# Performance work log

Hardware: AMD Instinct MI355X
Metric: run time of the kernel (lower is better)

## Reference

```python
import math
import jax, jax.numpy as jnp
import numpy as np

B, S, T = 32, 512, 180
D, F, L, H = 512, 2048, 6, 8
DH = D // H


def _pos_encoding(length, d):
    pos = np.arange(length, dtype=np.float32)[:, None]
    div = np.exp(np.arange(0, d, 2, dtype=np.float32) * (-math.log(10000.0) / d))
    pe = np.zeros((length, d), dtype=np.float32)
    pe[:, 0::2] = np.sin(pos * div)
    pe[:, 1::2] = np.cos(pos * div)
    return jnp.asarray(pe)


def _ln(x, scale, bias):
    mu = x.mean(-1, keepdims=True)
    var = ((x - mu) ** 2).mean(-1, keepdims=True)
    return (x - mu) * jax.lax.rsqrt(var + 1e-5) * scale + bias


def _mha(q_in, kv_in, w, b, causal=False):
    # w: [4, D, D] = (Wq, Wk, Wv, Wo); b: [4, D]
    b_, sq = q_in.shape[:2]
    q = (q_in @ w[0] + b[0]).reshape(b_, sq, H, DH)
    k = (kv_in @ w[1] + b[1]).reshape(b_, -1, H, DH)
    v = (kv_in @ w[2] + b[2]).reshape(b_, -1, H, DH)
    s = jnp.einsum('bqhd,bkhd->bhqk', q, k) / math.sqrt(DH)
    if causal:
        mask = jnp.tril(jnp.ones((sq, k.shape[1]), dtype=bool))
        s = jnp.where(mask, s, -1e9)
    a = jax.nn.softmax(s, axis=-1)
    o = jnp.einsum('bhqk,bkhd->bqhd', a, v).reshape(b_, sq, D)
    return o @ w[3] + b[3]


def _ffn(x, w1, b1, w2, b2):
    return jax.nn.relu(x @ w1 + b1) @ w2 + b2


def setup_inputs() -> dict:
    key = jax.random.key(0)
    ks = jax.random.split(key, 16)
    n = lambda k, shape: jax.random.normal(k, shape, jnp.float32) * 0.02
    return {
        'x': jax.random.normal(ks[0], (B, S, 2), jnp.float32),
        'y_cv_teacher': jax.random.normal(ks[1], (B, T, 1), jnp.float32),
        'src_proj_w': n(ks[2], (2, D)), 'src_proj_b': jnp.zeros((D,), jnp.float32),
        'tgt_proj_w': n(ks[3], (1, D)), 'tgt_proj_b': jnp.zeros((D,), jnp.float32),
        'enc_attn_w': n(ks[4], (L, 4, D, D)), 'enc_attn_b': jnp.zeros((L, 4, D), jnp.float32),
        'enc_ffn_w1': n(ks[5], (L, D, F)), 'enc_ffn_b1': jnp.zeros((L, F), jnp.float32),
        'enc_ffn_w2': n(ks[6], (L, F, D)), 'enc_ffn_b2': jnp.zeros((L, D), jnp.float32),
        'enc_ln_scale': jnp.ones((L, 2, D), jnp.float32), 'enc_ln_bias': jnp.zeros((L, 2, D), jnp.float32),
        'dec_self_w': n(ks[7], (L, 4, D, D)), 'dec_self_b': jnp.zeros((L, 4, D), jnp.float32),
        'dec_cross_w': n(ks[8], (L, 4, D, D)), 'dec_cross_b': jnp.zeros((L, 4, D), jnp.float32),
        'dec_ffn_w1': n(ks[9], (L, D, F)), 'dec_ffn_b1': jnp.zeros((L, F), jnp.float32),
        'dec_ffn_w2': n(ks[10], (L, F, D)), 'dec_ffn_b2': jnp.zeros((L, D), jnp.float32),
        'dec_ln_scale': jnp.ones((L, 3, D), jnp.float32), 'dec_ln_bias': jnp.zeros((L, 3, D), jnp.float32),
        'out_w': n(ks[11], (D, 1)), 'out_b': jnp.zeros((1,), jnp.float32),
    }


def reference(x, y_cv_teacher, src_proj_w, src_proj_b, tgt_proj_w, tgt_proj_b,
              enc_attn_w, enc_attn_b, enc_ffn_w1, enc_ffn_b1, enc_ffn_w2, enc_ffn_b2,
              enc_ln_scale, enc_ln_bias, dec_self_w, dec_self_b, dec_cross_w, dec_cross_b,
              dec_ffn_w1, dec_ffn_b1, dec_ffn_w2, dec_ffn_b2, dec_ln_scale, dec_ln_bias,
              out_w, out_b):
    pe = _pos_encoding(512, D)
    # encoder (post-norm, relu FFN, dropout disabled = eval semantics)
    h = x @ src_proj_w + src_proj_b + pe[: x.shape[1]]
    for i in range(L):
        h = _ln(h + _mha(h, h, enc_attn_w[i], enc_attn_b[i]), enc_ln_scale[i, 0], enc_ln_bias[i, 0])
        h = _ln(h + _ffn(h, enc_ffn_w1[i], enc_ffn_b1[i], enc_ffn_w2[i], enc_ffn_b2[i]),
                enc_ln_scale[i, 1], enc_ln_bias[i, 1])
    memory = h
    # teacher-forced decoder input: [start=0, y_cv_teacher[:-1]]
    tgt_in = jnp.concatenate([jnp.zeros((x.shape[0], 1, 1), x.dtype), y_cv_teacher[:, :-1, :]], axis=1)
    d = tgt_in @ tgt_proj_w + tgt_proj_b + pe[: tgt_in.shape[1]]
    for i in range(L):
        d = _ln(d + _mha(d, d, dec_self_w[i], dec_self_b[i], causal=True),
                dec_ln_scale[i, 0], dec_ln_bias[i, 0])
        d = _ln(d + _mha(d, memory, dec_cross_w[i], dec_cross_b[i]),
                dec_ln_scale[i, 1], dec_ln_bias[i, 1])
        d = _ln(d + _ffn(d, dec_ffn_w1[i], dec_ffn_b1[i], dec_ffn_w2[i], dec_ffn_b2[i]),
                dec_ln_scale[i, 2], dec_ln_bias[i, 2])
    return d @ out_w + out_b  # [B, T, 1]
```

## Files before the change

kernel.cpp:

```cpp
#include <hip/hip_runtime.h>
#include <math.h>

#define B_  32
#define S_  512
#define T_  180
#define D_  512
#define F_  2048
#define L_  6
#define H_  8
#define DH_ 64

typedef unsigned short u16;
typedef __attribute__((ext_vector_type(8))) short short8;
typedef __attribute__((ext_vector_type(4))) float floatx4;

__device__ __forceinline__ float bf2f(u16 h) {
    union { unsigned u; float f; } un; un.u = ((unsigned)h) << 16; return un.f;
}
__device__ __forceinline__ u16 f2bf(float f) {
    union { float f; unsigned u; } un; un.f = f;
    unsigned u = un.u;
    u += 0x7fffu + ((u >> 16) & 1u);
    return (u16)(u >> 16);
}
__device__ __forceinline__ unsigned cvt_pk_bf16(float lo, float hi) {
    unsigned r;
    asm("v_cvt_pk_bf16_f32 %0, %1, %2" : "=v"(r) : "v"(lo), "v"(hi));
    return r;
}

__device__ __forceinline__ void gload16(const u16* g, u16* l) {
    __builtin_amdgcn_global_load_lds(
        (const __attribute__((address_space(1))) void*)g,
        (__attribute__((address_space(3))) void*)l, 16, 0, 0);
}

__device__ __forceinline__ float pos_enc(int pos, int c) {
    int i2 = c & ~1;
    float div = expf(-(float)i2 * (9.210340371976184f / 512.0f));
    float arg = (float)pos * div;
    return (c & 1) ? cosf(arg) : sinf(arg);
}

__global__ __launch_bounds__(256) void embed_src_kernel(
    const float* __restrict__ x, const float* __restrict__ w,
    const float* __restrict__ b, u16* __restrict__ h)
{
    int idx = blockIdx.x * 256 + threadIdx.x;
    if (idx >= B_ * S_ * D_) return;
    int c  = idx & (D_ - 1);
    int bs = idx >> 9;
    int s  = bs & (S_ - 1);
    float x0 = x[bs * 2 + 0];
    float x1 = x[bs * 2 + 1];
    h[idx] = f2bf(x0 * w[c] + x1 * w[D_ + c] + b[c] + pos_enc(s, c));
}

__global__ __launch_bounds__(256) void embed_tgt_kernel(
    const float* __restrict__ y, const float* __restrict__ w,
    const float* __restrict__ b, u16* __restrict__ d)
{
    int idx = blockIdx.x * 256 + threadIdx.x;
    if (idx >= B_ * T_ * D_) return;
    int c  = idx & (D_ - 1);
    int bt = idx >> 9;
    int t  = bt % T_;
    int bb = bt / T_;
    float tv = (t == 0) ? 0.0f : y[bb * T_ + (t - 1)];
    d[idx] = f2bf(tv * w[c] + b[c] + pos_enc(t, c));
}

__global__ __launch_bounds__(256) void wconv_kernel(
    const float* __restrict__ W, u16* __restrict__ Wt, int K, int N)
{
    __shared__ float tile[32][33];
    size_t mat = (size_t)blockIdx.z * K * N;
    const float* Wm = W + mat;
    u16* Wtm = Wt + mat;
    int n0 = blockIdx.x * 32, k0 = blockIdx.y * 32;
    int tx = threadIdx.x & 31, ty = threadIdx.x >> 5;
#pragma unroll
    for (int i = 0; i < 32; i += 8)
        tile[ty + i][tx] = Wm[(size_t)(k0 + ty + i) * N + n0 + tx];
    __syncthreads();
#pragma unroll
    for (int i = 0; i < 32; i += 8)
        Wtm[(size_t)(n0 + ty + i) * K + k0 + tx] = f2bf(tile[tx][ty + i]);
}

__global__ __launch_bounds__(256) void gemm_bf16_kernel(
    const u16* __restrict__ A, int lda, const u16* __restrict__ Bt,
    const float* __restrict__ bias, u16* __restrict__ C, int ldc,
    int M, int N, int K, int relu)
{
    __shared__ u16 smem[18432];
    u16* As = smem;
    u16* Bs = smem + 8192;

    int tid  = threadIdx.x;
    int w    = tid >> 6;
    int lane = tid & 63;
    int m0 = blockIdx.y << 7, n0 = blockIdx.x << 7;

    int sr = w * 32 + (lane >> 2);
    int sk = (lane & 3) * 8;
    const u16* ag0 = A  + (size_t)(m0 + sr)      * lda + sk;
    const u16* ag1 = A  + (size_t)(m0 + sr + 16) * lda + sk;
    const u16* bg0 = Bt + (size_t)(n0 + sr)      * K + sk;
    const u16* bg1 = Bt + (size_t)(n0 + sr + 16) * K + sk;
    u16* al0 = As + (w * 2 + 0) * 512;
    u16* al1 = As + (w * 2 + 1) * 512;
    u16* bl0 = Bs + (w * 2 + 0) * 512;
    u16* bl1 = Bs + (w * 2 + 1) * 512;

    int wm = (w >> 1) * 64, wn = (w & 1) * 64;
    int fr = lane & 15;
    int fk = (lane >> 4) * 8;

    floatx4 acc[4][4] = {};

    for (int k0 = 0; k0 < K; k0 += 64) {
#pragma unroll
        for (int hh = 0; hh < 2; ++hh) {
            int go = k0 + hh * 32;
            int lo = hh * 4096;
            gload16(ag0 + go, al0 + lo);
            gload16(ag1 + go, al1 + lo);
            gload16(bg0 + go, bl0 + lo);
            gload16(bg1 + go, bl1 + lo);
        }
        __syncthreads();

#pragma unroll
        for (int hh = 0; hh < 2; ++hh) {
            int lo = hh * 4096;
            short8 af[4], bf[4];
#pragma unroll
            for (int i = 0; i < 4; ++i)
                af[i] = *(const short8*)&As[lo + (wm + i * 16 + fr) * 32 + fk];
#pragma unroll
            for (int j = 0; j < 4; ++j)
                bf[j] = *(const short8*)&Bs[lo + (wn + j * 16 + fr) * 32 + fk];
#pragma unroll
            for (int i = 0; i < 4; ++i)
#pragma unroll
                for (int j = 0; j < 4; ++j)
                    acc[i][j] = __builtin_amdgcn_mfma_f32_16x16x32_bf16(
                        af[i], bf[j], acc[i][j], 0, 0, 0);
        }
        __syncthreads();
    }

    u16* epi = smem + w * 4608;
    int cc = lane & 15;
    int rq = (lane >> 4) * 4;
#pragma unroll
    for (int j = 0; j < 4; ++j) {
        float bj = bias[n0 + wn + j * 16 + cc];
#pragma unroll
        for (int i = 0; i < 4; ++i) {
#pragma unroll
            for (int r = 0; r < 4; ++r) {
                float vv = acc[i][j][r] + bj;
                if (relu) vv = fmaxf(vv, 0.f);
                epi[(i * 16 + rq + r) * 72 + j * 16 + cc] = f2bf(vv);
            }
        }
    }
    __syncthreads();
#pragma unroll
    for (int t = 0; t < 8; ++t) {
        int er = t * 8 + (lane >> 3);
        int ec = (lane & 7) * 8;
        short8 vv = *(const short8*)&epi[er * 72 + ec];
        *(short8*)&C[(size_t)(m0 + wm + er) * ldc + n0 + wn + ec] = vv;
    }
}

#define SBAR()       asm volatile("s_barrier" ::: "memory")
#define WAIT_LGKM0() do { asm volatile("s_waitcnt lgkmcnt(0)" ::: "memory"); \
                          __builtin_amdgcn_sched_barrier(0); } while (0)
#define WAIT_VM(N)   asm volatile("s_waitcnt vmcnt(" #N ")" ::: "memory")

#define RD_A(BUF, MH) do { \
  _Pragma("unroll") for (int i_ = 0; i_ < 4; ++i_) \
  _Pragma("unroll") for (int h_ = 0; h_ < 2; ++h_) \
    a[i_][h_] = *(const short8*)&smem[(BUF) * 16384 + \
        ((MH) * 128 + qm + i_ * 16 + fr) * 64 + cSwz[h_]]; \
} while (0)

#define RD_B(BUF, NH) do { \
  _Pragma("unroll") for (int n_ = 0; n_ < 2; ++n_) \
  _Pragma("unroll") for (int h_ = 0; h_ < 2; ++h_) \
    bb[n_][h_] = *(const short8*)&smem[32768 + (BUF) * 16384 + \
        ((NH) * 128 + qn + n_ * 16 + fr) * 64 + cSwz[h_]]; \
} while (0)

#define PH_MMA(MH, NH) do { \
  __builtin_amdgcn_s_setprio(1); \
  _Pragma("unroll") for (int i_ = 0; i_ < 4; ++i_) \
  _Pragma("unroll") for (int n_ = 0; n_ < 2; ++n_) \
  _Pragma("unroll") for (int h_ = 0; h_ < 2; ++h_) \
    acc[MH][NH][i_][n_] = __builtin_amdgcn_mfma_f32_16x16x32_bf16( \
        a[i_][h_], bb[n_][h_], acc[MH][NH][i_][n_], 0, 0, 0); \
  __builtin_amdgcn_s_setprio(0); \
} while (0)

__global__ __launch_bounds__(512, 2) void gemm256_bf16_kernel(
    const u16* __restrict__ A, int lda, const u16* __restrict__ Bt,
    const float* __restrict__ bias, u16* __restrict__ C, int ldc,
    int M, int N, int K, int relu)
{
    __shared__ __align__(128) u16 smem[65536];
    const int AB0 = 0, AB1 = 16384, BB0 = 32768, BB1 = 49152;

    int tid = threadIdx.x;
    int w = tid >> 6, lane = tid & 63;
    int fr = lane & 15, q = lane >> 4;
    int qm = (w >> 2) * 64, qn = (w & 3) * 32;
    int r8 = tid >> 3;
    int ksrc = (((tid & 7) ^ (r8 & 7)) << 3);
    int cSwz[2];
    cSwz[0] = ((q ^ (fr & 7)) << 3);
    cSwz[1] = (((4 | q) ^ (fr & 7)) << 3);

    int nbx = gridDim.x;
    int nwg = nbx * gridDim.y;
    int flat = blockIdx.y * nbx + blockIdx.x;
    int qq = nwg >> 3, rr = nwg & 7;
    int xcd = flat & 7, sidx = flat >> 3;
    int wg = (xcd < rr ? xcd * (qq + 1) : rr * (qq + 1) + (xcd - rr) * qq) + sidx;
    int m0 = (wg / nbx) << 8, n0 = (wg % nbx) << 8;

    auto stg = [&](const u16* __restrict__ G, int ld, int row0, int bufOff,
                   int half, int gk) {
#pragma unroll
        for (int j = 0; j < 2; ++j) {
            int rl = half * 128 + j * 64 + r8;
            gload16(G + (size_t)(row0 + rl) * ld + gk + ksrc,
                    smem + bufOff + ((half * 128 + j * 64 + (w << 3)) << 6));
        }
    };

    short8 a[4][2], bb[2][2];
    floatx4 acc[2][2][4][2] = {};

    stg(A,  lda, m0, AB0, 0, 0);
    stg(A,  lda, m0, AB0, 1, 0);
    stg(Bt, K,   n0, BB0, 0, 0);
    stg(Bt, K,   n0, BB0, 1, 0);
    stg(Bt, K,   n0, BB1, 1, 64);
    stg(A,  lda, m0, AB1, 1, 64);
    WAIT_VM(4);
    SBAR();

    int NIT = K >> 7;
    for (int it = 0; it < NIT; ++it) {
        const int notlast = (it < NIT - 1);
        const int gk1 = it * 128 + 64, gk2 = gk1 + 64, gk3 = gk2 + 64;
        RD_A(0, 0); RD_B(0, 1);
        stg(A, lda, m0, AB1, 0, gk1);
        WAIT_LGKM0(); PH_MMA(0, 1); SBAR();
        RD_A(0, 1);
        stg(Bt, K, n0, BB1, 0, gk1);
        WAIT_LGKM0(); PH_MMA(1, 1); WAIT_VM(8); SBAR();
        RD_B(0, 0);
        if (notlast) stg(Bt, K, n0, BB0, 1, gk2);
        WAIT_LGKM0(); PH_MMA(1, 0); SBAR();
        RD_A(0, 0);
        if (notlast) stg(A, lda, m0, AB0, 1, gk2);
        WAIT_LGKM0(); PH_MMA(0, 0);
        if (notlast) { WAIT_VM(6); } else { WAIT_VM(2); }
        SBAR();
        RD_A(1, 0); RD_B(1, 1);
        if (notlast) stg(A, lda, m0, AB0, 0, gk2);
        WAIT_LGKM0(); PH_MMA(0, 1); SBAR();
        RD_A(1, 1);
        if (notlast) stg(Bt, K, n0, BB0, 0, gk2);
        WAIT_LGKM0(); PH_MMA(1, 1);
        if (notlast) { WAIT_VM(8); } else { WAIT_VM(0); }
        SBAR();
        RD_B(1, 0);
        if (notlast) stg(Bt, K, n0, BB1, 1, gk3);
        WAIT_LGKM0(); PH_MMA(1, 0); SBAR();
        RD_A(1, 0);
        if (notlast) stg(A, lda, m0, AB1, 1, gk3);
        WAIT_LGKM0(); PH_MMA(0, 0);
        if (notlast) WAIT_VM(6);
        SBAR();
    }

    u16* epi = smem + w * 2560;
    int rq = q * 4;
#pragma unroll
    for (int mh = 0; mh < 2; ++mh) {
#pragma unroll
        for (int nh = 0; nh < 2; ++nh) {
            __syncthreads();
            int bcol = n0 + nh * 128 + qn;
            int brow = m0 + mh * 128 + qm;
#pragma unroll
            for (int n = 0; n < 2; ++n) {
                float bj = bias[bcol + n * 16 + fr];
#pragma unroll
                for (int i = 0; i < 4; ++i)
#pragma unroll
                    for (int r = 0; r < 4; ++r) {
                        float vv = acc[mh][nh][i][n][r] + bj;
                        if (relu) vv = fmaxf(vv, 0.f);
                        epi[(i * 16 + rq + r) * 40 + n * 16 + fr] = f2bf(vv);
                    }
            }
            __syncthreads();
#pragma unroll
            for (int t = 0; t < 4; ++t) {
                int er = t * 16 + (lane >> 2);
                int ec = (lane & 3) * 8;
                short8 vv = *(const short8*)&epi[er * 40 + ec];
                *(short8*)&C[(size_t)(brow + er) * ldc + bcol + ec] = vv;
            }
        }
    }
}

#define CEXP 0.1803368801111244f

__global__ __launch_bounds__(256) void attn_mfma_kernel(
    const u16* Q, int qs, const u16* __restrict__ K, int ks,
    const u16* __restrict__ V, u16* O,
    int Sq, int Sk, int causal)
{
    __shared__ u16 Qs[4096];
    __shared__ u16 Ks[4096];
    __shared__ u16 Vt[64 * 72];
    __shared__ u16 Ps[4][16 * 72];

    int tid  = threadIdx.x;
    int w    = tid >> 6;
    int lane = tid & 63;
    int n    = lane & 15;
    int quad = lane >> 4;
    int bh = blockIdx.x;
    int bb = bh >> 3, hhd = bh & 7;
    int q0 = blockIdx.y * 64;

    const u16* Qb = Q + (size_t)bb * Sq * qs + hhd * DH_;
    const u16* Kb = K + (size_t)bb * Sk * ks + hhd * DH_;
    const u16* Vb = V + (size_t)bb * Sk * ks + hhd * DH_;

    int sr = tid >> 3;
    int gk = (((tid & 7) ^ (sr & 7)) << 3);

    gload16(Qb + (size_t)(q0 + sr) * qs + gk, Qs + tid * 8);
    gload16(Qb + (size_t)(q0 + 32 + sr) * qs + gk, Qs + 2048 + tid * 8);

    float m_i = -1e30f, l_i = 0.f;
    floatx4 o_acc[4] = {};
    int qg = q0 + w * 16 + n;
    int kend = causal ? ((Sk < q0 + 64) ? Sk : (q0 + 64)) : Sk;

    int csw0 = ((quad ^ (n & 7)) << 3);
    int csw1 = (((4 | quad) ^ (n & 7)) << 3);

    __syncthreads();

    short8 aq0 = *(const short8*)&Qs[(w * 16 + n) * 64 + csw0];
    short8 aq1 = *(const short8*)&Qs[(w * 16 + n) * 64 + csw1];

    for (int k0 = 0; k0 < kend; k0 += 64) {
        gload16(Kb + (size_t)(k0 + sr) * ks + gk, Ks + tid * 8);
        gload16(Kb + (size_t)(k0 + 32 + sr) * ks + gk, Ks + 2048 + tid * 8);
#pragma unroll
        for (int it = 0; it < 2; ++it) {
            int idx = it * 256 + tid;
            int r = idx >> 3, dg = (idx & 7) * 8;
            short8 vv = *(const short8*)&Vb[(size_t)(k0 + r) * ks + dg];
            int col = (r + dg) & 63;
#pragma unroll
            for (int j = 0; j < 8; ++j)
                Vt[(dg + j) * 72 + col] = (u16)vv[j];
        }
        __syncthreads();

        floatx4 sc[4] = {};
#pragma unroll
        for (int j = 0; j < 4; ++j) {
            short8 bk0 = *(const short8*)&Ks[(j * 16 + n) * 64 + csw0];
            short8 bk1 = *(const short8*)&Ks[(j * 16 + n) * 64 + csw1];
            sc[j] = __builtin_amdgcn_mfma_f32_16x16x32_bf16(bk0, aq0, sc[j], 0, 0, 0);
            sc[j] = __builtin_amdgcn_mfma_f32_16x16x32_bf16(bk1, aq1, sc[j], 0, 0, 0);
        }

        bool need_mask = (k0 + 64 > Sk) ||
                         (causal && (k0 + 63 > q0 + w * 16));
        if (need_mask) {
#pragma unroll
            for (int j = 0; j < 4; ++j) {
#pragma unroll
                for (int r = 0; r < 4; ++r) {
                    int kg = k0 + j * 16 + quad * 4 + r;
                    if (kg >= Sk || (causal && kg > qg))
                        sc[j][r] = -1e30f;
                }
            }
        }

        float mx = sc[0][0];
#pragma unroll
        for (int j = 0; j < 4; ++j)
#pragma unroll
            for (int r = 0; r < 4; ++r) mx = fmaxf(mx, sc[j][r]);
        mx = fmaxf(mx, __shfl_xor(mx, 16));
        mx = fmaxf(mx, __shfl_xor(mx, 32));
        if (__any(mx > m_i + 8.0f)) {
            float mnew = fmaxf(m_i, mx);
            float alpha = exp2f((m_i - mnew) * CEXP);
            m_i = mnew;
            l_i *= alpha;
#pragma unroll
            for (int jb = 0; jb < 4; ++jb)
#pragma unroll
                for (int r = 0; r < 4; ++r) o_acc[jb][r] *= alpha;
        }
        float ps = 0.f;
#pragma unroll
        for (int j = 0; j < 4; ++j)
#pragma unroll
            for (int r = 0; r < 4; ++r) {
                float p = exp2f((sc[j][r] - m_i) * CEXP);
                sc[j][r] = p; ps += p;
            }
        ps += __shfl_xor(ps, 16);
        ps += __shfl_xor(ps, 32);
        l_i += ps;

#pragma unroll
        for (int j = 0; j < 4; ++j) {
            unsigned p0 = cvt_pk_bf16(sc[j][0], sc[j][1]);
            unsigned p1 = cvt_pk_bf16(sc[j][2], sc[j][3]);
            *(uint2*)&Ps[w][n * 72 + j * 16 + quad * 4] = make_uint2(p0, p1);
        }

        short8 ap0 = *(const short8*)&Ps[w][n * 72 + quad * 8];
        short8 ap1 = *(const short8*)&Ps[w][n * 72 + 32 + quad * 8];
#pragma unroll
        for (int jb = 0; jb < 4; ++jb) {
            int d = jb * 16 + n;
            int rot = d & ~7;
            short8 bv0 = *(const short8*)&Vt[d * 72 + ((quad * 8 + rot) & 63)];
            short8 bv1 = *(const short8*)&Vt[d * 72 + ((32 + quad * 8 + rot) & 63)];
            o_acc[jb] = __builtin_amdgcn_mfma_f32_16x16x32_bf16(bv0, ap0, o_acc[jb], 0, 0, 0);
            o_acc[jb] = __builtin_amdgcn_mfma_f32_16x16x32_bf16(bv1, ap1, o_acc[jb], 0, 0, 0);
        }
        __syncthreads();
    }

    float inv = 1.0f / l_i;
    u16* Ob = O + (size_t)bb * Sq * qs + hhd * DH_;
    if (qg < Sq) {
#pragma unroll
        for (int jb = 0; jb < 4; ++jb) {
            unsigned p0 = cvt_pk_bf16(o_acc[jb][0] * inv, o_acc[jb][1] * inv);
            unsigned p1 = cvt_pk_bf16(o_acc[jb][2] * inv, o_acc[jb][3] * inv);
            *(uint2*)&Ob[(size_t)qg * qs + jb * 16 + quad * 4] = make_uint2(p0, p1);
        }
    }
}

__global__ __launch_bounds__(128) void add_ln_kernel(
    u16* __restrict__ h, const u16* __restrict__ delta,
    const float* __restrict__ scale, const float* __restrict__ bias)
{
    __shared__ float red[2][2];
    int row = blockIdx.x, tid = threadIdx.x;
    int lane = tid & 63, wv = tid >> 6;
    size_t base = (size_t)row * D_ + tid * 4;
    uint2 hv = *(const uint2*)&h[base];
    uint2 dv = *(const uint2*)&delta[base];
    float v0 = bf2f(hv.x & 0xffff) + bf2f(dv.x & 0xffff);
    float v1 = bf2f(hv.x >> 16)    + bf2f(dv.x >> 16);
    float v2 = bf2f(hv.y & 0xffff) + bf2f(dv.y & 0xffff);
    float v3 = bf2f(hv.y >> 16)    + bf2f(dv.y >> 16);

    float a  = v0 + v1 + v2 + v3;
    float b2 = v0 * v0 + v1 * v1 + v2 * v2 + v3 * v3;
#pragma unroll
    for (int off = 32; off > 0; off >>= 1) {
        a  += __shfl_xor(a, off);
        b2 += __shfl_xor(b2, off);
    }
    if (lane == 0) { red[wv][0] = a; red[wv][1] = b2; }
    __syncthreads();
    float S1 = red[0][0] + red[1][0];
    float S2 = red[0][1] + red[1][1];
    float mu = S1 * (1.0f / 512.0f);
    float var = S2 * (1.0f / 512.0f) - mu * mu;
    float rs = rsqrtf(var + 1e-5f);

    int c = tid * 4;
    float4 sc = *(const float4*)&scale[c];
    float4 bi = *(const float4*)&bias[c];
    unsigned lo = (unsigned)f2bf((v0 - mu) * rs * sc.x + bi.x) |
                  ((unsigned)f2bf((v1 - mu) * rs * sc.y + bi.y) << 16);
    unsigned hi = (unsigned)f2bf((v2 - mu) * rs * sc.z + bi.z) |
                  ((unsigned)f2bf((v3 - mu) * rs * sc.w + bi.w) << 16);
    *(uint2*)&h[base] = make_uint2(lo, hi);
}

__global__ __launch_bounds__(64) void out_proj_kernel(
    const u16* __restrict__ d, const float* __restrict__ w,
    const float* __restrict__ b, float* __restrict__ out)
{
    int row = blockIdx.x, lane = threadIdx.x;
    float s = 0.f;
    for (int c = lane; c < D_; c += 64) s += bf2f(d[(size_t)row * D_ + c]) * w[c];
#pragma unroll
    for (int off = 32; off > 0; off >>= 1) s += __shfl_down(s, off);
    if (lane == 0) out[row] = s + b[0];
}

extern "C" void kernel_launch(void* const* d_in, const int* in_sizes, int n_in,
                              void* d_out, int out_size, void* d_ws, size_t ws_size,
                              hipStream_t stream)
{
    const float* x          = (const float*)d_in[0];
    const float* y          = (const float*)d_in[1];
    const float* src_w      = (const float*)d_in[2];
    const float* src_b      = (const float*)d_in[3];
    const float* tgt_w      = (const float*)d_in[4];
    const float* tgt_b      = (const float*)d_in[5];
    const float* enc_attn_w = (const float*)d_in[6];
    const float* enc_attn_b = (const float*)d_in[7];
    const float* enc_ffn_w1 = (const float*)d_in[8];
    const float* enc_ffn_b1 = (const float*)d_in[9];
    const float* enc_ffn_w2 = (const float*)d_in[10];
    const float* enc_ffn_b2 = (const float*)d_in[11];
    const float* enc_ln_s   = (const float*)d_in[12];
    const float* enc_ln_b   = (const float*)d_in[13];
    const float* dec_self_w = (const float*)d_in[14];
    const float* dec_self_b = (const float*)d_in[15];
    const float* dec_cross_w= (const float*)d_in[16];
    const float* dec_cross_b= (const float*)d_in[17];
    const float* dec_ffn_w1 = (const float*)d_in[18];
    const float* dec_ffn_b1 = (const float*)d_in[19];
    const float* dec_ffn_w2 = (const float*)d_in[20];
    const float* dec_ffn_b2 = (const float*)d_in[21];
    const float* dec_ln_s   = (const float*)d_in[22];
    const float* dec_ln_b   = (const float*)d_in[23];
    const float* out_w      = (const float*)d_in[24];
    const float* out_b      = (const float*)d_in[25];
    float* out = (float*)d_out;

    const size_t E_BSD = (size_t)B_ * S_ * D_;
    const size_t E_BTD = (size_t)B_ * T_ * D_;
    const size_t WDD   = (size_t)D_ * D_;
    const size_t WDF   = (size_t)D_ * F_;
    const int MS = B_ * S_;
    const int MT = B_ * T_;
    const int MTP = 5888;

    u16* h    = (u16*)d_ws;
    u16* qkv  = h + E_BSD;
    u16* o    = qkv + (size_t)MS * 1536;
    u16* dbuf = o + E_BSD;
    u16* wsc  = dbuf + E_BTD;
    u16* mid  = qkv;
    u16* cq   = qkv;
    u16* ckv  = qkv + 4 * 1024 * 1024;

    auto gemm = [&](const u16* A, int lda, const u16* Wt, const float* bi,
                    u16* C, int ldc, int M, int N, int K, int relu) {
        dim3 g(N / 128, M / 128);
        gemm_bf16_kernel<<<g, dim3(256), 0, stream>>>(A, lda, Wt, bi, C, ldc,
                                                      M, N, K, relu);
    };
    auto gemm256 = [&](const u16* A, int lda, const u16* Wt, const float* bi,
                       u16* C, int ldc, int M, int N, int K, int relu) {
        dim3 g(N / 256, M / 256);
        gemm256_bf16_kernel<<<g, dim3(512), 0, stream>>>(A, lda, Wt, bi, C, ldc,
                                                         M, N, K, relu);
    };
    auto attn = [&](const u16* Qp, int qs, const u16* Kp, int ks,
                    const u16* Vp, u16* Op, int Sq, int Sk, int causal) {
        dim3 g(B_ * H_, (Sq + 63) / 64);
        attn_mfma_kernel<<<g, dim3(256), 0, stream>>>(Qp, qs, Kp, ks, Vp, Op,
                                                      Sq, Sk, causal);
    };
    auto addln = [&](u16* hp, const u16* dp, const float* sc, const float* bi,
                     int rows) {
        add_ln_kernel<<<dim3(rows), dim3(128), 0, stream>>>(hp, dp, sc, bi);
    };
    auto wconv = [&](const float* W, u16* Wt, int K, int N, int nmat) {
        wconv_kernel<<<dim3(N / 32, K / 32, nmat), dim3(256), 0, stream>>>(W, Wt, K, N);
    };

    embed_src_kernel<<<dim3((B_ * S_ * D_ + 255) / 256), dim3(256), 0, stream>>>(
        x, src_w, src_b, h);
    for (int l = 0; l < L_; ++l) {
        wconv(enc_attn_w + (size_t)l * 4 * WDD, wsc, D_, D_, 4);
        wconv(enc_ffn_w1 + (size_t)l * WDF, wsc + 4 * WDD, D_, F_, 1);
        wconv(enc_ffn_w2 + (size_t)l * WDF, wsc + 4 * WDD + WDF, F_, D_, 1);

        const float* bl = enc_attn_b + (size_t)l * 4 * D_;
        gemm256(h, D_, wsc, bl, qkv, 1536, MS, 1536, D_, 0);
        attn(qkv, 1536, qkv + 512, 1536, qkv + 1024, qkv, S_, S_, 0);
        gemm(qkv, 1536, wsc + 3 * WDD, bl + 3 * D_, o, D_, MS, D_, D_, 0);
        addln(h, o, enc_ln_s + (size_t)l * 2 * D_, enc_ln_b + (size_t)l * 2 * D_, MS);

        for (int m0 = 0; m0 < MS; m0 += 8192) {
            gemm256(h + (size_t)m0 * D_, D_, wsc + 4 * WDD,
                    enc_ffn_b1 + (size_t)l * F_, mid, F_, 8192, F_, D_, 1);
            gemm(mid, F_, wsc + 4 * WDD + WDF, enc_ffn_b2 + (size_t)l * D_,
                 o + (size_t)m0 * D_, D_, 8192, D_, F_, 0);
        }
        addln(h, o, enc_ln_s + (size_t)l * 2 * D_ + D_,
              enc_ln_b + (size_t)l * 2 * D_ + D_, MS);
    }

    embed_tgt_kernel<<<dim3((B_ * T_ * D_ + 255) / 256), dim3(256), 0, stream>>>(
        y, tgt_w, tgt_b, dbuf);
    for (int l = 0; l < L_; ++l) {
        wconv(dec_self_w  + (size_t)l * 4 * WDD, wsc, D_, D_, 4);
        wconv(dec_cross_w + (size_t)l * 4 * WDD, wsc + 4 * WDD, D_, D_, 4);
        wconv(dec_ffn_w1  + (size_t)l * WDF, wsc + 8 * WDD, D_, F_, 1);
        wconv(dec_ffn_w2  + (size_t)l * WDF, wsc + 8 * WDD + WDF, F_, D_, 1);

        const float* bl = dec_self_b + (size_t)l * 4 * D_;
        gemm256(dbuf, D_, wsc, bl, qkv, 1536, MTP, 1536, D_, 0);
        attn(qkv, 1536, qkv + 512, 1536, qkv + 1024, qkv, T_, T_, 1);
        gemm(qkv, 1536, wsc + 3 * WDD, bl + 3 * D_, o, D_, MT, D_, D_, 0);
        addln(dbuf, o, dec_ln_s + (size_t)l * 3 * D_,
              dec_ln_b + (size_t)l * 3 * D_, MT);

        const float* bc = dec_cross_b + (size_t)l * 4 * D_;
        gemm256(h, D_, wsc + 5 * WDD, bc + D_, ckv, 1024, MS, 1024, D_, 0);
        gemm(dbuf, D_, wsc + 4 * WDD, bc, cq, D_, MT, D_, D_, 0);
        attn(cq, 512, ckv, 1024, ckv + 512, cq, T_, S_, 0);
        gemm(cq, D_, wsc + 7 * WDD, bc + 3 * D_, o, D_, MT, D_, D_, 0);
        addln(dbuf, o, dec_ln_s + (size_t)l * 3 * D_ + D_,
              dec_ln_b + (size_t)l * 3 * D_ + D_, MT);

        gemm256(dbuf, D_, wsc + 8 * WDD, dec_ffn_b1 + (size_t)l * F_,
                mid, F_, MTP, F_, D_, 1);
        gemm(mid, F_, wsc + 8 * WDD + WDF, dec_ffn_b2 + (size_t)l * D_,
             o, D_, MT, D_, F_, 0);
        addln(dbuf, o, dec_ln_s + (size_t)l * 3 * D_ + 2 * D_,
              dec_ln_b + (size_t)l * 3 * D_ + 2 * D_, MT);
    }

    out_proj_kernel<<<dim3(MT), dim3(64), 0, stream>>>(dbuf, out_w, out_b, out);
}
```

Before: 3.192 ms.

## Fuse N=512 output GEMMs with residual add and LayerNorm into one kernel

Adds a gemm_ln kernel in which each block computes a full 64x512 row tile of the attention-output or FFN-down projection. It stages the tile through shared memory, then applies bias, residual add and LayerNorm before writing the result back into the hidden buffer. This replaces the separate gemm and add_ln launches and the intermediate round trip through the o buffer. In exchange, the new GEMM is a simpler double-buffered loop with a 64-row tile, so fewer blocks are launched (M/64) and the main loop may be less tuned than the original gemm kernel.

```diff
diff --git a/kernel.cpp b/kernel.cpp
--- a/kernel.cpp
+++ b/kernel.cpp
@@ -34,6 +34,11 @@
         (const __attribute__((address_space(1))) void*)g,
         (__attribute__((address_space(3))) void*)l, 16, 0, 0);
 }
+
+#define SBAR()       asm volatile("s_barrier" ::: "memory")
+#define WAIT_LGKM0() do { asm volatile("s_waitcnt lgkmcnt(0)" ::: "memory"); \
+                          __builtin_amdgcn_sched_barrier(0); } while (0)
+#define WAIT_VM(N)   asm volatile("s_waitcnt vmcnt(" #N ")" ::: "memory")
 
 __device__ __forceinline__ float pos_enc(int pos, int c) {
     int i2 = c & ~1;
@@ -176,11 +181,6 @@
         *(short8*)&C[(size_t)(m0 + wm + er) * ldc + n0 + wn + ec] = vv;
     }
 }
-
-#define SBAR()       asm volatile("s_barrier" ::: "memory")
-#define WAIT_LGKM0() do { asm volatile("s_waitcnt lgkmcnt(0)" ::: "memory"); \
-                          __builtin_amdgcn_sched_barrier(0); } while (0)
-#define WAIT_VM(N)   asm volatile("s_waitcnt vmcnt(" #N ")" ::: "memory")
 
 #define RD_A(BUF, MH) do { \
   _Pragma("unroll") for (int i_ = 0; i_ < 4; ++i_) \
@@ -323,6 +323,106 @@
     }
 }
 
+__global__ __launch_bounds__(256, 2) void gemm_ln_kernel(
+    const u16* __restrict__ A, int lda, const u16* __restrict__ Bt,
+    const float* __restrict__ gbias, u16* __restrict__ h,
+    const float* __restrict__ lscale, const float* __restrict__ lbias,
+    int K)
+{
+    __shared__ u16 smem[36864];
+    int tid = threadIdx.x;
+    int w = tid >> 6, lane = tid & 63;
+    int fr = lane & 15, quad = lane >> 4;
+    int wn = w * 128;
+    int m0 = blockIdx.x * 64;
+    int srow = tid >> 2, skk = (tid & 3) * 8;
+
+    const u16* Ab = A + (size_t)(m0 + srow) * lda + skk;
+    const u16* Bb = Bt + (size_t)srow * K + skk;
+
+    auto stage = [&](int buf, int k0) {
+        u16* s = smem + buf * 18432;
+        gload16(Ab + k0, s + tid * 8);
+#pragma unroll
+        for (int t = 0; t < 8; ++t)
+            gload16(Bb + (size_t)t * 64 * K + k0, s + 2048 + t * 2048 + tid * 8);
+    };
+
+    floatx4 acc[4][8] = {};
+    stage(0, 0);
+    int NIT = K >> 5;
+    for (int it = 0; it < NIT; ++it) {
+        int cur = it & 1;
+        if (it + 1 < NIT) { stage(cur ^ 1, (it + 1) << 5); WAIT_VM(9); }
+        else             { WAIT_VM(0); }
+        __syncthreads();
+        const u16* s = smem + cur * 18432;
+        short8 a[4], b[8];
+#pragma unroll
+        for (int i = 0; i < 4; ++i)
+            a[i] = *(const short8*)&s[(i * 16 + fr) * 32 + quad * 8];
+#pragma unroll
+        for (int j = 0; j < 8; ++j)
+            b[j] = *(const short8*)&s[2048 + (wn + j * 16 + fr) * 32 + quad * 8];
+#pragma unroll
+        for (int i = 0; i < 4; ++i)
+#pragma unroll
+            for (int j = 0; j < 8; ++j)
+                acc[i][j] = __builtin_amdgcn_mfma_f32_16x16x32_bf16(
+                    a[i], b[j], acc[i][j], 0, 0, 0);
+        __syncthreads();
+    }
+
+    u16* epi = smem;
+#pragma unroll
+    for (int j = 0; j < 8; ++j) {
+        float bj = gbias[wn + j * 16 + fr];
+#pragma unroll
+        for (int i = 0; i < 4; ++i)
+#pragma unroll
+            for (int r = 0; r < 4; ++r)
+                epi[(i * 16 + quad * 4 + r) * 516 + wn + j * 16 + fr] =
+                    f2bf(acc[i][j][r] + bj);
+    }
+    __syncthreads();
+
+    int row = tid >> 2, c0 = (tid & 3) * 128;
+    const u16* er = epi + row * 516 + c0;
+    u16* hr = h + (size_t)(m0 + row) * 512 + c0;
+    float s1 = 0.f, s2 = 0.f;
+#pragma unroll
+    for (int sb = 0; sb < 16; ++sb) {
+        short8 cv = *(const short8*)&er[sb * 8];
+        short8 hv = *(const short8*)&hr[sb * 8];
+#pragma unroll
+        for (int e = 0; e < 8; ++e) {
+            float v = bf2f((u16)cv[e]) + bf2f((u16)hv[e]);
+            s1 += v; s2 += v * v;
+        }
+    }
+    s1 += __shfl_xor(s1, 1, 4); s1 += __shfl_xor(s1, 2, 4);
+    s2 += __shfl_xor(s2, 1, 4); s2 += __shfl_xor(s2, 2, 4);
+    float mu = s1 * (1.0f / 512.0f);
+    float var = s2 * (1.0f / 512.0f) - mu * mu;
+    float rs = rsqrtf(var + 1e-5f);
+#pragma unroll
+    for (int sb = 0; sb < 16; ++sb) {
+        short8 cv = *(const short8*)&er[sb * 8];
+        short8 hv = *(const short8*)&hr[sb * 8];
+        unsigned ow[4];
+#pragma unroll
+        for (int p = 0; p < 4; ++p) {
+            int c = c0 + sb * 8 + p * 2;
+            float va = bf2f((u16)cv[p * 2])     + bf2f((u16)hv[p * 2]);
+            float vb = bf2f((u16)cv[p * 2 + 1]) + bf2f((u16)hv[p * 2 + 1]);
+            float ra = (va - mu) * rs * lscale[c]     + lbias[c];
+            float rb = (vb - mu) * rs * lscale[c + 1] + lbias[c + 1];
+            ow[p] = cvt_pk_bf16(ra, rb);
+        }
+        *(uint4*)&hr[sb * 8] = make_uint4(ow[0], ow[1], ow[2], ow[3]);
+    }
+}
+
 #define CEXP 0.1803368801111244f
 
 __global__ __launch_bounds__(256) void attn_mfma_kernel(
@@ -465,46 +565,6 @@
             *(uint2*)&Ob[(size_t)qg * qs + jb * 16 + quad * 4] = make_uint2(p0, p1);
         }
     }
-}
-
-__global__ __launch_bounds__(128) void add_ln_kernel(
-    u16* __restrict__ h, const u16* __restrict__ delta,
-    const float* __restrict__ scale, const float* __restrict__ bias)
-{
-    __shared__ float red[2][2];
-    int row = blockIdx.x, tid = threadIdx.x;
-    int lane = tid & 63, wv = tid >> 6;
-    size_t base = (size_t)row * D_ + tid * 4;
-    uint2 hv = *(const uint2*)&h[base];
-    uint2 dv = *(const uint2*)&delta[base];
-    float v0 = bf2f(hv.x & 0xffff) + bf2f(dv.x & 0xffff);
-    float v1 = bf2f(hv.x >> 16)    + bf2f(dv.x >> 16);
-    float v2 = bf2f(hv.y & 0xffff) + bf2f(dv.y & 0xffff);
-    float v3 = bf2f(hv.y >> 16)    + bf2f(dv.y >> 16);
-
-    float a  = v0 + v1 + v2 + v3;
-    float b2 = v0 * v0 + v1 * v1 + v2 * v2 + v3 * v3;
-#pragma unroll
-    for (int off = 32; off > 0; off >>= 1) {
-        a  += __shfl_xor(a, off);
-        b2 += __shfl_xor(b2, off);
-    }
-    if (lane == 0) { red[wv][0] = a; red[wv][1] = b2; }
-    __syncthreads();
-    float S1 = red[0][0] + red[1][0];
-    float S2 = red[0][1] + red[1][1];
-    float mu = S1 * (1.0f / 512.0f);
-    float var = S2 * (1.0f / 512.0f) - mu * mu;
-    float rs = rsqrtf(var + 1e-5f);
-
-    int c = tid * 4;
-    float4 sc = *(const float4*)&scale[c];
-    float4 bi = *(const float4*)&bias[c];
-    unsigned lo = (unsigned)f2bf((v0 - mu) * rs * sc.x + bi.x) |
-                  ((unsigned)f2bf((v1 - mu) * rs * sc.y + bi.y) << 16);
-    unsigned hi = (unsigned)f2bf((v2 - mu) * rs * sc.z + bi.z) |
-                  ((unsigned)f2bf((v3 - mu) * rs * sc.w + bi.w) << 16);
-    *(uint2*)&h[base] = make_uint2(lo, hi);
 }
 
 __global__ __launch_bounds__(64) void out_proj_kernel(
@@ -580,16 +640,17 @@
         gemm256_bf16_kernel<<<g, dim3(512), 0, stream>>>(A, lda, Wt, bi, C, ldc,
                                                          M, N, K, relu);
     };
+    auto gemmln = [&](const u16* A, int lda, const u16* Wt, const float* gb,
+                      u16* hp, const float* ls, const float* lb, int M, int K) {
+        gemm_ln_kernel<<<dim3(M / 64), dim3(256), 0, stream>>>(
+            A, lda, Wt, gb, hp, ls, lb, K);
+    };
     auto attn = [&](const u16* Qp, int qs, const u16* Kp, int ks,
                     const u16* Vp, u16* Op, int Sq, int Sk, int causal) {
         dim3 g(B_ * H_, (Sq + 63) / 64);
         attn_mfma_kernel<<<g, dim3(256), 0, stream>>>(Qp, qs, Kp, ks, Vp, Op,
                                                       Sq, Sk, causal);
     };
-    auto addln = [&](u16* hp, const u16* dp, const float* sc, const float* bi,
-                     int rows) {
-        add_ln_kernel<<<dim3(rows), dim3(128), 0, stream>>>(hp, dp, sc, bi);
-    };
     auto wconv = [&](const float* W, u16* Wt, int K, int N, int nmat) {
         wconv_kernel<<<dim3(N / 32, K / 32, nmat), dim3(256), 0, stream>>>(W, Wt, K, N);
     };
@@ -604,17 +665,18 @@
         const float* bl = enc_attn_b + (size_t)l * 4 * D_;
         gemm256(h, D_, wsc, bl, qkv, 1536, MS, 1536, D_, 0);
         attn(qkv, 1536, qkv + 512, 1536, qkv + 1024, qkv, S_, S_, 0);
-        gemm(qkv, 1536, wsc + 3 * WDD, bl + 3 * D_, o, D_, MS, D_, D_, 0);
-        addln(h, o, enc_ln_s + (size_t)l * 2 * D_, enc_ln_b + (size_t)l * 2 * D_, MS);
+        gemmln(qkv, 1536, wsc + 3 * WDD, bl + 3 * D_, h,
+               enc_ln_s + (size_t)l * 2 * D_, enc_ln_b + (size_t)l * 2 * D_,
+               MS, D_);
 
         for (int m0 = 0; m0 < MS; m0 += 8192) {
             gemm256(h + (size_t)m0 * D_, D_, wsc + 4 * WDD,
                     enc_ffn_b1 + (size_t)l * F_, mid, F_, 8192, F_, D_, 1);
-            gemm(mid, F_, wsc + 4 * WDD + WDF, enc_ffn_b2 + (size_t)l * D_,
-                 o + (size_t)m0 * D_, D_, 8192, D_, F_, 0);
-        }
-        addln(h, o, enc_ln_s + (size_t)l * 2 * D_ + D_,
-              enc_ln_b + (size_t)l * 2 * D_ + D_, MS);
+            gemmln(mid, F_, wsc + 4 * WDD + WDF, enc_ffn_b2 + (size_t)l * D_,
+                   h + (size_t)m0 * D_,
+                   enc_ln_s + (size_t)l * 2 * D_ + D_,
+                   enc_ln_b + (size_t)l * 2 * D_ + D_, 8192, F_);
+        }
     }
 
     embed_tgt_kernel<<<dim3((B_ * T_ * D_ + 255) / 256), dim3(256), 0, stream>>>(
@@ -628,24 +690,23 @@
         const float* bl = dec_self_b + (size_t)l * 4 * D_;
         gemm256(dbuf, D_, wsc, bl, qkv, 1536, MTP, 1536, D_, 0);
         attn(qkv, 1536, qkv + 512, 1536, qkv + 1024, qkv, T_, T_, 1);
-        gemm(qkv, 1536, wsc + 3 * WDD, bl + 3 * D_, o, D_, MT, D_, D_, 0);
-        addln(dbuf, o, dec_ln_s + (size_t)l * 3 * D_,
-              dec_ln_b + (size_t)l * 3 * D_, MT);
+        gemmln(qkv, 1536, wsc + 3 * WDD, bl + 3 * D_, dbuf,
+               dec_ln_s + (size_t)l * 3 * D_, dec_ln_b + (size_t)l * 3 * D_,
+               MT, D_);
 
         const float* bc = dec_cross_b + (size_t)l * 4 * D_;
         gemm256(h, D_, wsc + 5 * WDD, bc + D_, ckv, 1024, MS, 1024, D_, 0);
         gemm(dbuf, D_, wsc + 4 * WDD, bc, cq, D_, MT, D_, D_, 0);
         attn(cq, 512, ckv, 1024, ckv + 512, cq, T_, S_, 0);
-        gemm(cq, D_, wsc + 7 * WDD, bc + 3 * D_, o, D_, MT, D_, D_, 0);
-        addln(dbuf, o, dec_ln_s + (size_t)l * 3 * D_ + D_,
-              dec_ln_b + (size_t)l * 3 * D_ + D_, MT);
+        gemmln(cq, 512, wsc + 7 * WDD, bc + 3 * D_, dbuf,
+               dec_ln_s + (size_t)l * 3 * D_ + D_,
+               dec_ln_b + (size_t)l * 3 * D_ + D_, MT, D_);
 
         gemm256(dbuf, D_, wsc + 8 * WDD, dec_ffn_b1 + (size_t)l * F_,
                 mid, F_, MTP, F_, D_, 1);
-        gemm(mid, F_, wsc + 8 * WDD + WDF, dec_ffn_b2 + (size_t)l * D_,
-             o, D_, MT, D_, F_, 0);
-        addln(dbuf, o, dec_ln_s + (size_t)l * 3 * D_ + 2 * D_,
-              dec_ln_b + (size_t)l * 3 * D_ + 2 * D_, MT);
+        gemmln(mid, F_, wsc + 8 * WDD + WDF, dec_ffn_b2 + (size_t)l * D_,
+               dbuf, dec_ln_s + (size_t)l * 3 * D_ + 2 * D_,
+               dec_ln_b + (size_t)l * 3 * D_ + 2 * D_, MT, F_);
     }
 
     out_proj_kernel<<<dim3(MT), dim3(64), 0, stream>>>(dbuf, out_w, out_b, out);
```

Measured after the change: 4.030 ms. +26.2%, slower.
